# Optimization experiments

Hardware: AMD Instinct MI355X
Metric: run time of the kernel (lower is better)

Reference implementation:

```python
import jax, jax.numpy as jnp
import numpy as np

B, NMAX, T, FIN, H, K, OUT = 64, 256, 16, 3, 32, 8, 64
N = B * NMAX            # 16384 total nodes
EPG = 2048              # edges per graph
E = B * EPG             # 131072 edges
EPS = 1e-15


def gcn_conv(x, src, dst, ew, W, b):
    # x: [N, T, FIN] -> [N, T, H]; GCNConv: symmetric norm with self-loops (weight 1)
    xw = jnp.einsum('ntf,fh->nth', x, W)
    loops = jnp.arange(N, dtype=src.dtype)
    src_a = jnp.concatenate([src, loops])
    dst_a = jnp.concatenate([dst, loops])
    w_a = jnp.concatenate([ew, jnp.ones((N,), ew.dtype)])
    deg = jax.ops.segment_sum(w_a, dst_a, num_segments=N)
    dinv = jnp.where(deg > 0, jax.lax.rsqrt(deg), 0.0)
    norm = dinv[src_a] * w_a * dinv[dst_a]
    out = jax.ops.segment_sum(xw[src_a] * norm[:, None, None], dst_a, num_segments=N)
    return out + b


def dense_mincut_pool(x, adj, s):
    # x [B,T,Nc,H], adj [B,Nc,Nc], s [B,Nc,Kc]  (mask is all-True: equal-size graphs)
    s = jax.nn.softmax(s, axis=-1)
    kc = s.shape[-1]
    out = jnp.einsum('bnk,btnh->btkh', s, x)
    out_adj = jnp.einsum('bnk,bnm,bml->bkl', s, adj, s)
    mincut_num = jnp.trace(out_adj, axis1=-2, axis2=-1)
    d_flat = adj.sum(-1)
    mincut_den = jnp.einsum('bnk,bn,bnk->b', s, d_flat, s)
    mincut_loss = -jnp.mean(mincut_num / mincut_den)
    ss = jnp.einsum('bnk,bnl->bkl', s, s)
    i_s = jnp.eye(kc, dtype=x.dtype)
    ss_n = jnp.linalg.norm(ss, axis=(-2, -1), keepdims=True)
    ortho_loss = jnp.mean(jnp.linalg.norm(ss / ss_n - i_s / jnp.sqrt(kc), axis=(-2, -1)))
    out_adj = out_adj * (1.0 - i_s)  # zero diagonal
    d = jnp.sqrt(out_adj.sum(-1))[:, None, :] + EPS  # [B,1,K]
    out_adj = out_adj / d / jnp.swapaxes(d, 1, 2)
    return out, out_adj, mincut_loss, ortho_loss


def dense_graph_conv(x, adj, Wrel, brel, Wroot):
    # DenseGraphConv(aggr='add'): lin_rel(adj @ x) + lin_root(x)
    agg = jnp.einsum('bnm,btmh->btnh', adj, x)
    return jnp.einsum('btnh,ho->btno', agg, Wrel) + brel + jnp.einsum('btnh,ho->btno', x, Wroot)


def _forward(pos, edge_attr, W1, b1, Wp1, bp1, Wrel2, brel2, Wroot2, Wp2, bp2,
             Wrel3, brel3, Wroot3, Wp3, bp3, Wrel4, brel4, Wroot4, edge_src, edge_dst):
    x = jax.nn.relu(gcn_conv(pos, edge_src, edge_dst, edge_attr, W1, b1))  # [N,T,H]
    # to_dense_batch (equal-size graphs => reshape) then transpose(1,2)
    xd = x.reshape(B, NMAX, T, H).transpose(0, 2, 1, 3)  # [B,T,NMAX,H]
    gb = edge_src // NMAX
    adj = jnp.zeros((B, NMAX, NMAX), jnp.float32).at[gb, edge_src % NMAX, edge_dst % NMAX].add(1.0)
    s1 = jnp.tanh((jnp.einsum('btnh,hk->btnk', xd, Wp1) + bp1).mean(1))   # [B,NMAX,8K]
    x1, adj1, mc1, o1 = dense_mincut_pool(xd, adj, s1)
    x1 = dense_graph_conv(x1, adj1, Wrel2, brel2, Wroot2)
    s2 = jnp.tanh((jnp.einsum('btnh,hk->btnk', x1, Wp2) + bp2).mean(1))   # [B,8K,4K]
    x2, adj2, mc2, o2 = dense_mincut_pool(x1, adj1, s2)
    x2 = dense_graph_conv(x2, adj2, Wrel3, brel3, Wroot3)
    s3 = jnp.tanh((jnp.einsum('btnh,hk->btnk', x2, Wp3) + bp3).mean(1))   # [B,4K,K]
    x3, adj3, mc3, o3 = dense_mincut_pool(x2, adj2, s3)
    x3 = dense_graph_conv(x3, adj3, Wrel4, brel4, Wroot4)                 # [B,T,K,OUT]
    p1 = jax.nn.softmax(s1, -1)
    p2 = jax.nn.softmax(s2, -1)
    p3 = jax.nn.softmax(s3, -1)
    agg = jnp.einsum('bnk,bkl,blm->bnm', p1, p2, p3)                       # [B,NMAX,K]
    return x3, mc1 + mc2 + mc3, o1 + o2 + o3, agg


def setup_inputs():
    key = jax.random.key(0)
    ks = jax.random.split(key, 16)
    pos = jax.random.normal(ks[0], (N, T, FIN), jnp.float32)
    gid = jnp.repeat(jnp.arange(B, dtype=jnp.int32), EPG)
    sl = jax.random.randint(ks[1], (E,), 0, NMAX, jnp.int32)
    dl = jax.random.randint(ks[2], (E,), 0, NMAX, jnp.int32)
    edge_src = gid * NMAX + sl
    edge_dst = gid * NMAX + dl
    edge_attr = jax.random.uniform(ks[3], (E,), jnp.float32)

    def lin(k, i, o):
        return jax.random.normal(k, (i, o), jnp.float32) / np.sqrt(i)

    return dict(
        pos=pos, edge_attr=edge_attr, edge_src=edge_src, edge_dst=edge_dst,
        W1=lin(ks[4], FIN, H), b1=jnp.zeros((H,), jnp.float32),
        Wp1=lin(ks[5], H, 8 * K), bp1=jnp.zeros((8 * K,), jnp.float32),
        Wrel2=lin(ks[6], H, H), brel2=jnp.zeros((H,), jnp.float32), Wroot2=lin(ks[7], H, H),
        Wp2=lin(ks[8], H, 4 * K), bp2=jnp.zeros((4 * K,), jnp.float32),
        Wrel3=lin(ks[9], H, H), brel3=jnp.zeros((H,), jnp.float32), Wroot3=lin(ks[10], H, H),
        Wp3=lin(ks[11], H, K), bp3=jnp.zeros((K,), jnp.float32),
        Wrel4=lin(ks[12], H, OUT), brel4=jnp.zeros((OUT,), jnp.float32), Wroot4=lin(ks[13], H, OUT),
    )


def reference(pos, edge_attr, edge_src, edge_dst, W1, b1, Wp1, bp1, Wrel2, brel2, Wroot2,
              Wp2, bp2, Wrel3, brel3, Wroot3, Wp3, bp3, Wrel4, brel4, Wroot4):
    return _forward(pos, edge_attr, W1, b1, Wp1, bp1, Wrel2, brel2, Wroot2, Wp2, bp2,
                    Wrel3, brel3, Wroot3, Wp3, bp3, Wrel4, brel4, Wroot4, edge_src, edge_dst)
```

## Files before the change

kernel.cpp:

```cpp
#include <hip/hip_runtime.h>
#include <math.h>

#define NB 64
#define TC 16
#define HC 32
#define NNODES 16384
#define NEDGES 131072
#define EPG 2048
#define EPSV 1e-15f

static inline int GRID(int n) { return (n + 255) / 256; }

template<int V> struct Log2 { static constexpr int v = 1 + Log2<V/2>::v; };
template<> struct Log2<1> { static constexpr int v = 0; };

__device__ inline float blk_sum256(float v, float* rbuf) {
    for (int o = 32; o > 0; o >>= 1) v += __shfl_xor(v, o);
    __syncthreads();
    if ((threadIdx.x & 63) == 0) rbuf[threadIdx.x >> 6] = v;
    __syncthreads();
    return rbuf[0] + rbuf[1] + rbuf[2] + rbuf[3];
}

__device__ inline float blk_sum512(float v, float* rbuf) {
    for (int o = 32; o > 0; o >>= 1) v += __shfl_xor(v, o);
    __syncthreads();
    if ((threadIdx.x & 63) == 0) rbuf[threadIdx.x >> 6] = v;
    __syncthreads();
    float s = 0.f;
#pragma unroll
    for (int i = 0; i < 8; ++i) s += rbuf[i];
    return s;
}

__global__ __launch_bounds__(512) void k_front(
        const int* __restrict__ esrc, const int* __restrict__ edst,
        const float* __restrict__ ea, const float* __restrict__ pos,
        const float* __restrict__ W1, const float* __restrict__ b1,
        const float* __restrict__ Wp1, const float* __restrict__ bp1,
        float* __restrict__ z, float* __restrict__ dinv_g,
        float* __restrict__ p1, float* __restrict__ mc) {
    __shared__ float dinvs[256];
    __shared__ __align__(16) float as_[1152];
    __shared__ __align__(16) float bs[1536];
    __shared__ __align__(16) float zs[1536];
    __shared__ float xm[1024];
    __shared__ float s1[2048];
    __shared__ __align__(16) float wp[2048];
    __shared__ float W1s[96];
    __shared__ float b1s[32];
    __shared__ float bp1s[64];

    int bid = blockIdx.x;
    int b = (bid & 7) * 8 + (bid >> 6);
    int dtile = ((bid >> 3) & 7) * 32;
    int tid = threadIdx.x;
    if (bid == 0 && tid < 2) mc[tid] = 0.f;
    ((float4*)wp)[tid] = ((const float4*)Wp1)[tid];
    if (tid < 96) W1s[tid] = W1[tid];
    if (tid < 32) b1s[tid] = b1[tid];
    if (tid < 64) bp1s[tid] = bp1[tid];

    int ebase = b * EPG;
    int svr[4], dvr[4];
    float evr[4];
#pragma unroll
    for (int j = 0; j < 4; ++j) {
        int e = ebase + tid + j * 512;
        svr[j] = esrc[e] & 255;
        dvr[j] = edst[e] & 255;
        evr[j] = ea[e];
    }
    if (tid < 256) dinvs[tid] = 1.0f;
    __syncthreads();
#pragma unroll
    for (int j = 0; j < 4; ++j) atomicAdd(&dinvs[dvr[j]], evr[j]);
    __syncthreads();
    float dvv = 0.f;
    if (tid < 256) {
        float dg = dinvs[tid];
        dvv = (dg > 0.f) ? rsqrtf(dg) : 0.f;
    }
    __syncthreads();
    if (tid < 256) dinvs[tid] = dvv;
    __syncthreads();
    if (dtile == 0 && tid < 256) dinv_g[b * 256 + tid] = dinvs[tid];

    int d = tid >> 4, q = tid & 15;
    bool act = (q < 12);
    float4 acc = make_float4(0.f, 0.f, 0.f, 0.f);
    const float* pbase = pos + (size_t)b * 256 * 48;
    for (int s0 = 0; s0 < 256; s0 += 32) {
        for (int i = tid; i < 288; i += 512)
            ((float4*)as_)[i] = make_float4(0.f, 0.f, 0.f, 0.f);
        __syncthreads();
#pragma unroll
        for (int j = 0; j < 4; ++j) {
            int dr = dvr[j] - dtile, sc = svr[j] - s0;
            if ((unsigned)dr < 32u && (unsigned)sc < 32u)
                atomicAdd(&as_[dr * 36 + sc], evr[j]);
        }
        for (int i = tid; i < 384; i += 512) {
            int r = i / 12, c = i % 12;
            float4 v = *(const float4*)(pbase + (size_t)(s0 + r) * 48 + c * 4);
            float dd = dinvs[s0 + r];
            v.x *= dd; v.y *= dd; v.z *= dd; v.w *= dd;
            *(float4*)(bs + r * 48 + c * 4) = v;
        }
        __syncthreads();
        if (act) {
#pragma unroll 8
            for (int sp = 0; sp < 32; ++sp) {
                float a = as_[d * 36 + sp];
                float4 bv = *(const float4*)&bs[sp * 48 + q * 4];
                acc.x += a * bv.x;
                acc.y += a * bv.y;
                acc.z += a * bv.z;
                acc.w += a * bv.w;
            }
        }
        __syncthreads();
    }
    if (act) {
        float dd = dinvs[dtile + d];
        float d2 = dd * dd;
        size_t goff = ((size_t)(b * 256 + dtile + d)) * 48 + q * 4;
        float4 pv = *(const float4*)(pos + goff);
        float4 zv;
        zv.x = acc.x * dd; zv.y = acc.y * dd; zv.z = acc.z * dd; zv.w = acc.w * dd;
        *(float4*)(z + goff) = zv;
        float4 av;
        av.x = zv.x + pv.x * d2;
        av.y = zv.y + pv.y * d2;
        av.z = zv.z + pv.z * d2;
        av.w = zv.w + pv.w * d2;
        *(float4*)&zs[d * 48 + q * 4] = av;
    }
    __syncthreads();
    {
        int h = tid & 31, ng = tid >> 5;
        float w0 = W1s[h], w1 = W1s[32 + h], w2 = W1s[64 + h], bb = b1s[h];
#pragma unroll
        for (int j = 0; j < 2; ++j) {
            int nn = ng * 2 + j;
            float a = 0.f;
#pragma unroll
            for (int t = 0; t < 16; ++t) {
                const float* ap = &zs[nn * 48 + t * 3];
                float y = fmaxf(ap[0] * w0 + ap[1] * w1 + ap[2] * w2 + bb, 0.f);
                a += y;
            }
            xm[nn * 32 + h] = a * (1.0f / 16.0f);
        }
    }
    __syncthreads();
    for (int i = tid; i < 2048; i += 512) {
        int n = i >> 6, k = i & 63;
        float a = bp1s[k];
#pragma unroll 8
        for (int h2 = 0; h2 < 32; ++h2) a += xm[n * 32 + h2] * wp[h2 * 64 + k];
        s1[i] = tanhf(a);
    }
    __syncthreads();
    {
        int wid = tid >> 6, lane = tid & 63;
        for (int r0 = wid; r0 < 32; r0 += 8) {
            float v = s1[r0 * 64 + lane];
            float m = v;
            for (int o = 32; o > 0; o >>= 1) m = fmaxf(m, __shfl_xor(m, o));
            float e = expf(v - m);
            float s = e;
            for (int o = 32; o > 0; o >>= 1) s += __shfl_xor(s, o);
            p1[((size_t)b * 256 + dtile + r0) * 64 + lane] = e / s;
        }
    }
}

__global__ __launch_bounds__(256) void k_pool1f(
        const float* __restrict__ z, const float* __restrict__ pos,
        const float* __restrict__ dinv, const float* __restrict__ p1,
        const float* __restrict__ W1, const float* __restrict__ b1,
        float* __restrict__ X1A) {
    __shared__ __align__(16) float ps[4096];
    __shared__ __align__(16) float ys[4096];
    __shared__ float zc[384];
    __shared__ float pc[384];
    __shared__ float dv[64];
    __shared__ float W1s[96];
    __shared__ float b1s[32];
    int bid = blockIdx.x;
    int b = (bid & 7) * 8 + (bid >> 6);
    int t0 = ((bid >> 3) & 7) * 2;
    int tid = threadIdx.x;
    if (tid < 96) W1s[tid] = W1[tid];
    if (tid < 32) b1s[tid] = b1[tid];
    __syncthreads();
    int hh = tid & 31;
    float w0 = W1s[hh], w1 = W1s[32 + hh], w2 = W1s[64 + hh], bb = b1s[hh];
    int th = tid >> 7, r = tid & 127;
    int k0 = (r >> 3) * 4, h0 = (r & 7) * 4;
    float acc[4][4];
#pragma unroll
    for (int a = 0; a < 4; ++a)
#pragma unroll
        for (int c = 0; c < 4; ++c) acc[a][c] = 0.f;
    for (int n0 = 0; n0 < 256; n0 += 64) {
        for (int i = tid; i < 1024; i += 256)
            ((float4*)ps)[i] = ((const float4*)(p1 + ((size_t)b * 256 + n0) * 64))[i];
        if (tid < 192) {
            int n = tid / 3, c = tid % 3;
            size_t off = ((size_t)(b * 256 + n0 + n)) * 48 + t0 * 3 + c * 2;
            *(float2*)&zc[n * 6 + c * 2] = *(const float2*)(z + off);
            *(float2*)&pc[n * 6 + c * 2] = *(const float2*)(pos + off);
        }
        if (tid < 64) dv[tid] = dinv[b * 256 + n0 + tid];
        __syncthreads();
        int g = tid >> 5;
#pragma unroll
        for (int j = 0; j < 16; ++j) {
            int pidx = g * 16 + j;
            int t = pidx >> 6, nn = pidx & 63;
            float d2 = dv[nn] * dv[nn];
            const float* zp = &zc[nn * 6 + t * 3];
            const float* pp = &pc[nn * 6 + t * 3];
            float a0 = zp[0] + pp[0] * d2;
            float a1 = zp[1] + pp[1] * d2;
            float a2 = zp[2] + pp[2] * d2;
            ys[t * 2048 + nn * 32 + hh] = fmaxf(a0 * w0 + a1 * w1 + a2 * w2 + bb, 0.f);
        }
        __syncthreads();
#pragma unroll 4
        for (int n = 0; n < 64; ++n) {
            float4 kv4 = *(const float4*)&ps[n * 64 + k0];
            float4 xv4 = *(const float4*)&ys[th * 2048 + n * 32 + h0];
            float kv[4] = {kv4.x, kv4.y, kv4.z, kv4.w};
            float xv[4] = {xv4.x, xv4.y, xv4.z, xv4.w};
#pragma unroll
            for (int a = 0; a < 4; ++a)
#pragma unroll
                for (int c = 0; c < 4; ++c) acc[a][c] += kv[a] * xv[c];
        }
        __syncthreads();
    }
    float* ob = X1A + (((size_t)(b * 16 + t0 + th) * 64 + k0) * 32 + h0);
#pragma unroll
    for (int a = 0; a < 4; ++a) {
        float4 v = {acc[a][0], acc[a][1], acc[a][2], acc[a][3]};
        *(float4*)(ob + (size_t)a * 32) = v;
    }
}

__global__ void k_adjp2(const int* __restrict__ esrc, const int* __restrict__ edst,
                        const float* __restrict__ p, float* __restrict__ tmp,
                        float* __restrict__ dflat) {
    __shared__ __align__(16) float as_[32 * 260];
    __shared__ __align__(16) float ps[64 * 64];
    int bid = blockIdx.x;
    int b = (bid & 7) * 8 + (bid >> 6);
    int nt0 = ((bid >> 3) & 7) * 32;
    int tid = threadIdx.x;
    for (int i = tid; i < 32 * 260 / 4; i += 256)
        ((float4*)as_)[i] = make_float4(0.f, 0.f, 0.f, 0.f);
    __syncthreads();
    int ebase = b * EPG;
#pragma unroll
    for (int j = 0; j < 8; ++j) {
        int e = ebase + tid + j * 256;
        int sv = esrc[e] & 255;
        int nr = sv - nt0;
        if ((unsigned)nr < 32u)
            atomicAdd(&as_[nr * 260 + (edst[e] & 255)], 1.0f);
    }
    __syncthreads();
    int n = tid >> 3, l0 = (tid & 7) * 8;
    float acc[8];
#pragma unroll
    for (int j = 0; j < 8; ++j) acc[j] = 0.f;
    float rs = 0.f;
    for (int m0 = 0; m0 < 256; m0 += 64) {
        for (int i = tid; i < 64 * 64 / 4; i += 256)
            ((float4*)ps)[i] = ((const float4*)(p + ((size_t)b * 256 + m0) * 64))[i];
        __syncthreads();
#pragma unroll 4
        for (int m = 0; m < 64; ++m) {
            float av = as_[n * 260 + m0 + m];
            rs += av;
            float4 p0 = *(const float4*)&ps[m * 64 + l0];
            float4 p1v = *(const float4*)&ps[m * 64 + l0 + 4];
            acc[0] += av * p0.x; acc[1] += av * p0.y; acc[2] += av * p0.z; acc[3] += av * p0.w;
            acc[4] += av * p1v.x; acc[5] += av * p1v.y; acc[6] += av * p1v.z; acc[7] += av * p1v.w;
        }
        __syncthreads();
    }
#pragma unroll
    for (int j = 0; j < 8; ++j)
        tmp[((size_t)b * 256 + nt0 + n) * 64 + l0 + j] = acc[j];
    if ((tid & 7) == 0) dflat[(size_t)b * 256 + nt0 + n] = rs;
}

template<int NC, int KC, int NSPLIT, int KT, int LT>
__global__ void k_ssgp(const float* __restrict__ p, const float* __restrict__ tmp,
                       const float* __restrict__ dflat, float* __restrict__ G,
                       float* __restrict__ Gden) {
    constexpr int NCH = NC / NSPLIT;
    constexpr int LC = 2 * KC;
    constexpr int KQ = KC / 4;
    __shared__ __align__(16) float ab[NCH * LC];
    __shared__ float rbuf[4];
    int bid = blockIdx.x;
    int idx = bid >> 3;
    int b = (bid & 7) * 8 + idx / NSPLIT;
    int split = idx % NSPLIT;
    int n0 = split * NCH;
    int tid = threadIdx.x;
    const float* pb = p + ((size_t)b * NC + n0) * KC;
    const float* tb = tmp + ((size_t)b * NC + n0) * KC;
    const float* db = dflat + (size_t)b * NC + n0;
    for (int i = tid; i < NCH * KQ; i += 256) {
        int r = i / KQ, c = i % KQ;
        *(float4*)(ab + r * LC + c * 4) = ((const float4*)pb)[i];
        *(float4*)(ab + r * LC + KC + c * 4) = ((const float4*)tb)[i];
    }
    __syncthreads();
    float den = 0.f;
    for (int i = tid; i < NCH * KQ; i += 256) {
        int r = i / KQ, c = i % KQ;
        float4 v = *(const float4*)(ab + r * LC + c * 4);
        den += (v.x * v.x + v.y * v.y + v.z * v.z + v.w * v.w) * db[r];
    }
    int kt = tid >> 4, lt = tid & 15;
    int k0 = kt * KT, l0 = lt * LT;
    float acc[KT][LT];
#pragma unroll
    for (int r = 0; r < KT; ++r)
#pragma unroll
        for (int c = 0; c < LT; ++c) acc[r][c] = 0.f;
#pragma unroll 4
    for (int n = 0; n < NCH; ++n) {
        float kv[KT], lv[LT];
#pragma unroll
        for (int r = 0; r < KT; ++r) kv[r] = ab[n * LC + k0 + r];
#pragma unroll
        for (int c = 0; c < LT; ++c) lv[c] = ab[n * LC + l0 + c];
#pragma unroll
        for (int r = 0; r < KT; ++r)
#pragma unroll
            for (int c = 0; c < LT; ++c) acc[r][c] += kv[r] * lv[c];
    }
    float* Gb = G + ((size_t)split * NB + b) * (KC * LC);
#pragma unroll
    for (int r = 0; r < KT; ++r)
#pragma unroll
        for (int c = 0; c < LT; ++c)
            Gb[(k0 + r) * LC + l0 + c] = acc[r][c];
    float dt = blk_sum256(den, rbuf);
    if (tid == 0) Gden[(size_t)split * NB + b] = dt;
}

__global__ __launch_bounds__(512) void k_tail_a(
        const float* __restrict__ X1A, const float* __restrict__ GBUF1,
        const float* __restrict__ GDEN1, const float* __restrict__ p1,
        const float* __restrict__ Wrel2, const float* __restrict__ brel2,
        const float* __restrict__ Wroot2,
        const float* __restrict__ Wp2, const float* __restrict__ bp2,
        const float* __restrict__ Wrel3, const float* __restrict__ brel3,
        const float* __restrict__ Wroot3,
        const float* __restrict__ Wp3, const float* __restrict__ bp3,
        float* __restrict__ OADJ1G, float* __restrict__ P2G,
        float* __restrict__ OADJ2G, float* __restrict__ P3G,
        float* __restrict__ OADJ3G, float* __restrict__ outagg,
        float* __restrict__ mc_out, float* __restrict__ or_out) {
    __shared__ __align__(16) float lds[16160];
    float* P2     = lds;
    float* XM2    = lds + 2304;
    float* OADJ2L = lds + 4608;
    float* P3L    = lds + 5760;
    float* OADJ3L = lds + 6016;
    float* DF3    = lds + 6080;
    float* DVV    = lds + 6112;
    float* RBUF   = lds + 6152;
    float* OADJ1s = lds + 6160;
    float* S      = lds + 10512;
    float* DF2    = lds + 16080;

    int bid = blockIdx.x;
    int b = ((bid & 7) << 3) | (bid >> 3);
    int tid = threadIdx.x;

    {
        float* FS = lds;
        float* FO = lds + 4160;
        float* FD = lds + 8320;
        float* FR = lds + 8384;
#pragma unroll
        for (int j = 0; j < 8; ++j) {
            int i = tid + j * 512;
            int k = i >> 6, l = i & 63;
            float sv = 0.f, ov = 0.f;
#pragma unroll
            for (int s = 0; s < 4; ++s) {
                const float* Gb = GBUF1 + ((size_t)s * NB + b) * 8192;
                sv += Gb[k * 128 + l];
                ov += Gb[k * 128 + 64 + l];
            }
            FS[k * 65 + l] = sv;
            FO[k * 65 + l] = ov;
        }
        __syncthreads();
        float ssn2 = 0.f;
#pragma unroll
        for (int j = 0; j < 8; ++j) {
            int i = tid + j * 512;
            float v = FS[(i >> 6) * 65 + (i & 63)];
            ssn2 += v * v;
        }
        float num = 0.f;
        if (tid < 64) num = FO[tid * 65 + tid];
        float den_t = 0.f;
#pragma unroll
        for (int s = 0; s < 4; ++s) den_t += GDEN1[(size_t)s * NB + b];
        float ssn2_t = blk_sum512(ssn2, FR);
        float num_t = blk_sum512(num, FR);
        float inv = 1.0f / sqrtf(ssn2_t);
        float dk = rsqrtf(64.0f);
        float o2 = 0.f;
#pragma unroll
        for (int j = 0; j < 8; ++j) {
            int i = tid + j * 512;
            int k = i >> 6, l = i & 63;
            float v = FS[k * 65 + l] * inv - ((k == l) ? dk : 0.f);
            o2 += v * v;
        }
        float o2_t = blk_sum512(o2, FR);
        if (tid == 0) {
            atomicAdd(mc_out, -(num_t / den_t) * (1.0f / NB));
            atomicAdd(or_out, sqrtf(o2_t) * (1.0f / NB));
        }
        if (tid < 64) {
            float rs = 0.f;
            for (int l = 0; l < 64; ++l) rs += FO[tid * 65 + l];
            rs -= FO[tid * 65 + tid];
            FD[tid] = sqrtf(rs) + EPSV;
        }
        __syncthreads();
        float ov8[8];
#pragma unroll
        for (int j = 0; j < 8; ++j) {
            int i = tid + j * 512;
            int k = i >> 6, l = i & 63;
            ov8[j] = (k == l) ? 0.f : FO[k * 65 + l] / (FD[k] * FD[l]);
        }
        __syncthreads();
#pragma unroll
        for (int j = 0; j < 8; ++j) {
            int i = tid + j * 512;
            int k = i >> 6, l = i & 63;
            OADJ1s[k * 68 + l] = ov8[j];
            OADJ1G[(size_t)b * 4096 + i] = ov8[j];
        }
        __syncthreads();
        if (tid < 64) {
            float rs = 0.f;
            for (int l = 0; l < 64; ++l) rs += OADJ1s[tid * 68 + l];
            DF2[tid] = rs;
        }
        __syncthreads();
    }

    float* XM1A = S;
    for (int i = tid; i < 2048; i += 512) {
        float s = 0.f;
        for (int t = 0; t < 16; ++t) s += X1A[((size_t)b * 16 + t) * 2048 + i];
        XM1A[(i >> 5) * 36 + (i & 31)] = s * (1.0f / 16.0f);
    }
    {
        float* WR = P2;
        float* WO = P2 + 1024;
        for (int i = tid; i < 1024; i += 512) { WR[i] = Wrel2[i]; WO[i] = Wroot2[i]; }
        __syncthreads();
        float* C1 = S + 2304;
        int n = tid >> 3, j0 = (tid & 7) * 4;
        float a4[4] = {0, 0, 0, 0};
        for (int m = 0; m < 64; ++m) {
            float av = OADJ1s[n * 68 + m];
            float4 xv = *(const float4*)&XM1A[m * 36 + j0];
            a4[0] += av * xv.x; a4[1] += av * xv.y; a4[2] += av * xv.z; a4[3] += av * xv.w;
        }
        __syncthreads();
#pragma unroll
        for (int j = 0; j < 4; ++j) C1[n * 36 + j0 + j] = a4[j];
        __syncthreads();
        float o4[4];
#pragma unroll
        for (int j = 0; j < 4; ++j) o4[j] = brel2[j0 + j];
        for (int h = 0; h < 32; ++h) {
            float c1v = C1[n * 36 + h];
            float xav = XM1A[n * 36 + h];
            float4 wr = *(const float4*)&WR[h * 32 + j0];
            float4 wo = *(const float4*)&WO[h * 32 + j0];
            o4[0] += c1v * wr.x + xav * wo.x;
            o4[1] += c1v * wr.y + xav * wo.y;
            o4[2] += c1v * wr.z + xav * wo.z;
            o4[3] += c1v * wr.w + xav * wo.w;
        }
        __syncthreads();
#pragma unroll
        for (int j = 0; j < 4; ++j) XM2[n * 36 + j0 + j] = o4[j];
        __syncthreads();
    }
    {
        float* S2 = S;
        float* WP2s = S + 2048;
        for (int i = tid; i < 1024; i += 512) WP2s[i] = Wp2[i];
        __syncthreads();
        for (int i = tid; i < 2048; i += 512) {
            int n = i >> 5, k = i & 31;
            float a = bp2[k];
            for (int h = 0; h < 32; ++h) a += XM2[n * 36 + h] * WP2s[h * 32 + k];
            S2[i] = tanhf(a);
        }
        __syncthreads();
        int lane = tid & 31, rr = tid >> 5;
        for (int r0 = 0; r0 < 64; r0 += 16) {
            int row = r0 + rr;
            float v = S2[row * 32 + lane];
            float m = v;
            for (int o = 16; o > 0; o >>= 1) m = fmaxf(m, __shfl_xor(m, o, 32));
            float e = expf(v - m);
            float s = e;
            for (int o = 16; o > 0; o >>= 1) s += __shfl_xor(s, o, 32);
            P2[row * 36 + lane] = e / s;
        }
        __syncthreads();
        for (int i = tid; i < 2048; i += 512)
            P2G[(size_t)b * 2048 + i] = P2[(i >> 5) * 36 + (i & 31)];
    }
    float* TMP2 = S;
    {
        int n = tid >> 3, l0 = (tid & 7) * 4;
        float a4[4] = {0, 0, 0, 0};
        for (int m = 0; m < 64; ++m) {
            float av = OADJ1s[n * 68 + m];
            float4 pv = *(const float4*)&P2[m * 36 + l0];
            a4[0] += av * pv.x; a4[1] += av * pv.y; a4[2] += av * pv.z; a4[3] += av * pv.w;
        }
        __syncthreads();
#pragma unroll
        for (int j = 0; j < 4; ++j) TMP2[n * 36 + l0 + j] = a4[j];
        __syncthreads();
    }
    {
        float* GS = S + 2304;
        float* GO = S + 3360;
        int k = tid >> 4, l0 = (tid & 15) * 2;
        float as2[2] = {0, 0}, ao2[2] = {0, 0};
        for (int n = 0; n < 64; ++n) {
            float pv = P2[n * 36 + k];
            float2 lp = *(const float2*)&P2[n * 36 + l0];
            float2 lt = *(const float2*)&TMP2[n * 36 + l0];
            as2[0] += pv * lp.x; as2[1] += pv * lp.y;
            ao2[0] += pv * lt.x; ao2[1] += pv * lt.y;
        }
        GS[k * 33 + l0] = as2[0]; GS[k * 33 + l0 + 1] = as2[1];
        GO[k * 33 + l0] = ao2[0]; GO[k * 33 + l0 + 1] = ao2[1];
        __syncthreads();
        float den = 0.f;
        for (int i = tid; i < 2048; i += 512) {
            float pv = P2[(i >> 5) * 36 + (i & 31)];
            den += pv * pv * DF2[i >> 5];
        }
        float ssn2 = 0.f;
        for (int i = tid; i < 1024; i += 512) {
            float v = GS[(i >> 5) * 33 + (i & 31)];
            ssn2 += v * v;
        }
        float num = 0.f;
        if (tid < 32) num = GO[tid * 33 + tid];
        float den_t = blk_sum512(den, RBUF);
        float ssn2_t = blk_sum512(ssn2, RBUF);
        float num_t = blk_sum512(num, RBUF);
        float inv = 1.0f / sqrtf(ssn2_t);
        float dk = rsqrtf(32.0f);
        float o2 = 0.f;
        for (int i = tid; i < 1024; i += 512) {
            int kk = i >> 5, ll = i & 31;
            float v = GS[kk * 33 + ll] * inv - ((kk == ll) ? dk : 0.f);
            o2 += v * v;
        }
        float o2_t = blk_sum512(o2, RBUF);
        if (tid == 0) {
            atomicAdd(mc_out, -(num_t / den_t) * (1.0f / NB));
            atomicAdd(or_out, sqrtf(o2_t) * (1.0f / NB));
        }
        if (tid < 32) {
            float rs = 0.f;
            for (int l = 0; l < 32; ++l) rs += GO[tid * 33 + l];
            rs -= GO[tid * 33 + tid];
            DVV[tid] = sqrtf(rs) + EPSV;
        }
        __syncthreads();
        for (int i = tid; i < 1024; i += 512) {
            int kk = i >> 5, ll = i & 31;
            float v = (kk == ll) ? 0.f : GO[kk * 33 + ll] / (DVV[kk] * DVV[ll]);
            OADJ2L[kk * 36 + ll] = v;
            OADJ2G[(size_t)b * 1024 + i] = v;
        }
        __syncthreads();
        if (tid < 32) {
            float s = 0.f;
            for (int l = 0; l < 32; ++l) s += OADJ2L[tid * 36 + l];
            DF3[tid] = s;
        }
        __syncthreads();
    }
    float* XM2A = S;
    {
        int k = tid >> 4, h0 = (tid & 15) * 2;
        float a2[2] = {0, 0};
        for (int n = 0; n < 64; ++n) {
            float pv = P2[n * 36 + k];
            float2 xv = *(const float2*)&XM2[n * 36 + h0];
            a2[0] += pv * xv.x; a2[1] += pv * xv.y;
        }
        __syncthreads();
        XM2A[k * 36 + h0] = a2[0];
        XM2A[k * 36 + h0 + 1] = a2[1];
        __syncthreads();
    }
    float* XM2B = S + 4352;
    {
        float* WREL3s = S + 1152;
        float* WROOT3s = S + 2176;
        float* C1 = S + 3200;
        for (int i = tid; i < 1024; i += 512) {
            WREL3s[i] = Wrel3[i];
            WROOT3s[i] = Wroot3[i];
        }
        __syncthreads();
        int n = tid >> 4, j0 = (tid & 15) * 2;
        float a2[2] = {0, 0};
        for (int m = 0; m < 32; ++m) {
            float av = OADJ2L[n * 36 + m];
            float2 xv = *(const float2*)&XM2A[m * 36 + j0];
            a2[0] += av * xv.x; a2[1] += av * xv.y;
        }
        __syncthreads();
        C1[n * 36 + j0] = a2[0];
        C1[n * 36 + j0 + 1] = a2[1];
        __syncthreads();
        float o2v[2];
        o2v[0] = brel3[j0]; o2v[1] = brel3[j0 + 1];
        for (int h = 0; h < 32; ++h) {
            float c1v = C1[n * 36 + h];
            float xav = XM2A[n * 36 + h];
            float2 wr = *(const float2*)&WREL3s[h * 32 + j0];
            float2 wo = *(const float2*)&WROOT3s[h * 32 + j0];
            o2v[0] += c1v * wr.x + xav * wo.x;
            o2v[1] += c1v * wr.y + xav * wo.y;
        }
        __syncthreads();
        XM2B[n * 36 + j0] = o2v[0];
        XM2B[n * 36 + j0 + 1] = o2v[1];
        __syncthreads();
    }
    {
        float* WP3s = S;
        for (int i = tid; i < 256; i += 512) WP3s[i] = Wp3[i];
        __syncthreads();
        if (tid < 256) {
            int n = tid >> 3, kk = tid & 7;
            float a = bp3[kk];
            for (int h = 0; h < 32; ++h) a += XM2B[n * 36 + h] * WP3s[h * 8 + kk];
            float v = tanhf(a);
            float m = v;
            for (int o = 4; o > 0; o >>= 1) m = fmaxf(m, __shfl_xor(m, o, 8));
            float e = expf(v - m);
            float s = e;
            for (int o = 4; o > 0; o >>= 1) s += __shfl_xor(s, o, 8);
            P3L[n * 8 + kk] = e / s;
        }
        __syncthreads();
        if (tid < 256) P3G[(size_t)b * 256 + tid] = P3L[tid];
        __syncthreads();
    }
    {
        float* TMP3 = S;
        float* GS3 = S + 256;
        float* GO3 = S + 336;
        if (tid < 256) {
            int n = tid >> 3, l = tid & 7;
            float a = 0.f;
            for (int m = 0; m < 32; ++m) a += OADJ2L[n * 36 + m] * P3L[m * 8 + l];
            TMP3[n * 8 + l] = a;
        }
        __syncthreads();
        if (tid < 64) {
            int k = tid >> 3, ll = tid & 7;
            float accs = 0.f, acco = 0.f;
            for (int nn = 0; nn < 32; ++nn) {
                float pv = P3L[nn * 8 + k];
                accs += pv * P3L[nn * 8 + ll];
                acco += pv * TMP3[nn * 8 + ll];
            }
            GS3[k * 9 + ll] = accs;
            GO3[k * 9 + ll] = acco;
        }
        __syncthreads();
        float den = 0.f;
        if (tid < 256) {
            float pv = P3L[tid];
            den = pv * pv * DF3[tid >> 3];
        }
        float ssn2 = 0.f;
        if (tid < 64) {
            float v = GS3[(tid >> 3) * 9 + (tid & 7)];
            ssn2 = v * v;
        }
        float num = 0.f;
        if (tid < 8) num = GO3[tid * 9 + tid];
        float den_t = blk_sum512(den, RBUF);
        float ssn2_t = blk_sum512(ssn2, RBUF);
        float num_t = blk_sum512(num, RBUF);
        float inv = 1.0f / sqrtf(ssn2_t);
        float dk = rsqrtf(8.0f);
        float o2 = 0.f;
        if (tid < 64) {
            int k = tid >> 3, ll = tid & 7;
            float v = GS3[k * 9 + ll] * inv - ((k == ll) ? dk : 0.f);
            o2 = v * v;
        }
        float o2_t = blk_sum512(o2, RBUF);
        if (tid == 0) {
            atomicAdd(mc_out, -(num_t / den_t) * (1.0f / NB));
            atomicAdd(or_out, sqrtf(o2_t) * (1.0f / NB));
        }
        if (tid < 8) {
            float rs = 0.f;
            for (int ll = 0; ll < 8; ++ll) rs += GO3[tid * 9 + ll];
            rs -= GO3[tid * 9 + tid];
            DVV[32 + tid] = sqrtf(rs) + EPSV;
        }
        __syncthreads();
        if (tid < 64) {
            int k = tid >> 3, ll = tid & 7;
            float v = (k == ll) ? 0.f : GO3[k * 9 + ll] / (DVV[32 + k] * DVV[32 + ll]);
            OADJ3L[tid] = v;
            OADJ3G[(size_t)b * 64 + tid] = v;
        }
        __syncthreads();
    }
    {
        float* Q = S;
        {
            int k = tid >> 3, m = tid & 7;
            float a = 0.f;
            for (int l = 0; l < 32; ++l) a += P2[k * 36 + l] * P3L[l * 8 + m];
            Q[tid] = a;
        }
        __syncthreads();
        int row = tid >> 1, m0 = (tid & 1) * 4;
        const float* p1r = p1 + ((size_t)b * 256 + row) * 64;
        float a4[4] = {0, 0, 0, 0};
        for (int k = 0; k < 64; ++k) {
            float pv = p1r[k];
#pragma unroll
            for (int m = 0; m < 4; ++m) a4[m] += pv * Q[k * 8 + m0 + m];
        }
#pragma unroll
        for (int m = 0; m < 4; ++m)
            outagg[((size_t)b * 256 + row) * 8 + m0 + m] = a4[m];
    }
}

__global__ __launch_bounds__(256) void k_tail_b(
        const float* __restrict__ X1A, const float* __restrict__ oadj1,
        const float* __restrict__ P2G, const float* __restrict__ OADJ2G,
        const float* __restrict__ P3G, const float* __restrict__ OADJ3G,
        const float* __restrict__ Wrel2, const float* __restrict__ brel2,
        const float* __restrict__ Wroot2,
        const float* __restrict__ Wrel3, const float* __restrict__ brel3,
        const float* __restrict__ Wroot3,
        const float* __restrict__ Wrel4, const float* __restrict__ brel4,
        const float* __restrict__ Wroot4,
        float* __restrict__ outx) {
    __shared__ float A[13408];
    float* X1AT = A;
    float* OADJ1s = A + 2304;
    float* WrelS = A + 6656;
    float* WrootS = A + 7680;
    float* C1a = A + 8704;
    float* X1B = A + 11008;
    int bid = blockIdx.x;
    int idxg = bid >> 3;
    int t = idxg & 15;
    int b = (bid & 7) * 8 + (idxg >> 4);
    int bt = b * 16 + t;
    int tid = threadIdx.x;
    for (int i = tid; i < 2048; i += 256)
        X1AT[(i >> 5) * 36 + (i & 31)] = X1A[(size_t)bt * 2048 + i];
    for (int i = tid; i < 4096; i += 256)
        OADJ1s[(i >> 6) * 68 + (i & 63)] = oadj1[(size_t)b * 4096 + i];
    for (int i = tid; i < 1024; i += 256) {
        WrelS[i] = Wrel2[i];
        WrootS[i] = Wroot2[i];
    }
    __syncthreads();
    {
        int n = tid >> 2, j0 = (tid & 3) * 8;
        float a8[8];
#pragma unroll
        for (int j = 0; j < 8; ++j) a8[j] = 0.f;
        for (int m = 0; m < 64; ++m) {
            float av = OADJ1s[n * 68 + m];
            float4 x1 = *(const float4*)&X1AT[m * 36 + j0];
            float4 x2 = *(const float4*)&X1AT[m * 36 + j0 + 4];
            a8[0] += av * x1.x; a8[1] += av * x1.y; a8[2] += av * x1.z; a8[3] += av * x1.w;
            a8[4] += av * x2.x; a8[5] += av * x2.y; a8[6] += av * x2.z; a8[7] += av * x2.w;
        }
        __syncthreads();
#pragma unroll
        for (int j = 0; j < 8; ++j) C1a[n * 36 + j0 + j] = a8[j];
        __syncthreads();
        float o8[8];
#pragma unroll
        for (int j = 0; j < 8; ++j) o8[j] = brel2[j0 + j];
        for (int h = 0; h < 32; ++h) {
            float c1v = C1a[n * 36 + h];
            float xav = X1AT[n * 36 + h];
            float4 wr1 = *(const float4*)&WrelS[h * 32 + j0];
            float4 wr2 = *(const float4*)&WrelS[h * 32 + j0 + 4];
            float4 wo1 = *(const float4*)&WrootS[h * 32 + j0];
            float4 wo2 = *(const float4*)&WrootS[h * 32 + j0 + 4];
            o8[0] += c1v * wr1.x + xav * wo1.x; o8[1] += c1v * wr1.y + xav * wo1.y;
            o8[2] += c1v * wr1.z + xav * wo1.z; o8[3] += c1v * wr1.w + xav * wo1.w;
            o8[4] += c1v * wr2.x + xav * wo2.x; o8[5] += c1v * wr2.y + xav * wo2.y;
            o8[6] += c1v * wr2.z + xav * wo2.z; o8[7] += c1v * wr2.w + xav * wo2.w;
        }
        __syncthreads();
#pragma unroll
        for (int j = 0; j < 8; ++j) X1B[n * 36 + j0 + j] = o8[j];
        __syncthreads();
    }
    float* P2s = A;
    float* X2A = A + 2304;
    for (int i = tid; i < 2048; i += 256)
        P2s[(i >> 5) * 36 + (i & 31)] = P2G[(size_t)b * 2048 + i];
    __syncthreads();
    {
        int k = tid >> 3, h0 = (tid & 7) * 4;
        float a4[4] = {0, 0, 0, 0};
        for (int n = 0; n < 64; ++n) {
            float pv = P2s[n * 36 + k];
            float4 xv = *(const float4*)&X1B[n * 36 + h0];
            a4[0] += pv * xv.x; a4[1] += pv * xv.y; a4[2] += pv * xv.z; a4[3] += pv * xv.w;
        }
        __syncthreads();
        *(float4*)&X2A[k * 36 + h0] = make_float4(a4[0], a4[1], a4[2], a4[3]);
        __syncthreads();
    }
    float* OADJ2s = A + 3456;
    float* Wrel3s = A + 4608;
    float* Wroot3s = A + 5632;
    float* C1b = A + 6656;
    float* X2B = A + 7808;
    for (int i = tid; i < 1024; i += 256) {
        OADJ2s[(i >> 5) * 36 + (i & 31)] = OADJ2G[(size_t)b * 1024 + i];
        Wrel3s[i] = Wrel3[i];
        Wroot3s[i] = Wroot3[i];
    }
    __syncthreads();
    {
        int n = tid >> 3, j0 = (tid & 7) * 4;
        float a4[4] = {0, 0, 0, 0};
        for (int m = 0; m < 32; ++m) {
            float av = OADJ2s[n * 36 + m];
            float4 xv = *(const float4*)&X2A[m * 36 + j0];
            a4[0] += av * xv.x; a4[1] += av * xv.y; a4[2] += av * xv.z; a4[3] += av * xv.w;
        }
        __syncthreads();
        *(float4*)&C1b[n * 36 + j0] = make_float4(a4[0], a4[1], a4[2], a4[3]);
        __syncthreads();
        float o4[4];
#pragma unroll
        for (int j = 0; j < 4; ++j) o4[j] = brel3[j0 + j];
        for (int h = 0; h < 32; ++h) {
            float c1v = C1b[n * 36 + h];
            float xav = X2A[n * 36 + h];
            float4 wr = *(const float4*)&Wrel3s[h * 32 + j0];
            float4 wo = *(const float4*)&Wroot3s[h * 32 + j0];
            o4[0] += c1v * wr.x + xav * wo.x;
            o4[1] += c1v * wr.y + xav * wo.y;
            o4[2] += c1v * wr.z + xav * wo.z;
            o4[3] += c1v * wr.w + xav * wo.w;
        }
        __syncthreads();
        *(float4*)&X2B[n * 36 + j0] = make_float4(o4[0], o4[1], o4[2], o4[3]);
        __syncthreads();
    }
    float* P3s = A;
    float* X3A = A + 8960;
    P3s[tid] = P3G[(size_t)b * 256 + tid];
    __syncthreads();
    {
        int k = tid >> 5, h = tid & 31;
        float a = 0.f;
        for (int n = 0; n < 32; ++n) a += P3s[n * 8 + k] * X2B[n * 36 + h];
        __syncthreads();
        X3A[k * 36 + h] = a;
        __syncthreads();
    }
    {
        float* OADJ3s = A + 256;
        float* C3 = A + 320;
        float* Wrel4s = A + 9248;
        float* Wroot4s = A + 11296;
        if (tid < 64) OADJ3s[tid] = OADJ3G[(size_t)b * 64 + tid];
        for (int i = tid; i < 2048; i += 256) {
            Wrel4s[i] = Wrel4[i];
            Wroot4s[i] = Wroot4[i];
        }
        __syncthreads();
        int n = tid >> 5, h = tid & 31;
        float a = 0.f;
#pragma unroll
        for (int m = 0; m < 8; ++m) a += OADJ3s[n * 8 + m] * X3A[m * 36 + h];
        C3[n * 36 + h] = a;
        __syncthreads();
        int o0 = (tid & 31) * 2;
        float a0 = brel4[o0], a1 = brel4[o0 + 1];
        for (int hh = 0; hh < 32; ++hh) {
            float c3v = C3[n * 36 + hh];
            float x3v = X3A[n * 36 + hh];
            a0 += c3v * Wrel4s[hh * 64 + o0] + x3v * Wroot4s[hh * 64 + o0];
            a1 += c3v * Wrel4s[hh * 64 + o0 + 1] + x3v * Wroot4s[hh * 64 + o0 + 1];
        }
        float* ob = outx + ((size_t)bt * 8 + n) * 64 + o0;
        ob[0] = a0;
        ob[1] = a1;
    }
}


extern "C" void kernel_launch(void* const* d_in, const int* in_sizes, int n_in,
                              void* d_out, int out_size, void* d_ws, size_t ws_size,
                              hipStream_t stream) {
    const float* pos    = (const float*)d_in[0];
    const float* ea     = (const float*)d_in[1];
    const int*   esrc   = (const int*)d_in[2];
    const int*   edst   = (const int*)d_in[3];
    const float* W1     = (const float*)d_in[4];
    const float* b1     = (const float*)d_in[5];
    const float* Wp1    = (const float*)d_in[6];
    const float* bp1    = (const float*)d_in[7];
    const float* Wrel2  = (const float*)d_in[8];
    const float* brel2  = (const float*)d_in[9];
    const float* Wroot2 = (const float*)d_in[10];
    const float* Wp2    = (const float*)d_in[11];
    const float* bp2    = (const float*)d_in[12];
    const float* Wrel3  = (const float*)d_in[13];
    const float* brel3  = (const float*)d_in[14];
    const float* Wroot3 = (const float*)d_in[15];
    const float* Wp3    = (const float*)d_in[16];
    const float* bp3    = (const float*)d_in[17];
    const float* Wrel4  = (const float*)d_in[18];
    const float* brel4  = (const float*)d_in[19];
    const float* Wroot4 = (const float*)d_in[20];
    float* out = (float*)d_out;

    char* w = (char*)d_ws;
    float* TMP    = (float*)(w);
    float* GBUF1  = (float*)(w + 4194304);
    float* X1A    = (float*)(w + 12582912);
    float* Z      = (float*)(w + 20971520);
    float* P1     = (float*)(w + 25165824);
    float* DINV   = (float*)(w + 29360128);
    float* DFLAT  = (float*)(w + 29425664);
    float* GDEN1  = (float*)(w + 29507584);
    float* OADJ1  = (float*)(w + 29622272);
    float* P2G    = (float*)(w + 30670848);
    float* OADJ2G = (float*)(w + 31195136);
    float* P3G    = (float*)(w + 31457280);
    float* OADJ3G = (float*)(w + 31522816);
    float* MC     = out + 524288;

    k_front<<<NB * 8, 512, 0, stream>>>(esrc, edst, ea, pos, W1, b1, Wp1, bp1,
                                        Z, DINV, P1, MC);
    k_pool1f<<<NB * 8, 256, 0, stream>>>(Z, pos, DINV, P1, W1, b1, X1A);
    k_adjp2<<<NB * 8, 256, 0, stream>>>(esrc, edst, P1, TMP, DFLAT);
    k_ssgp<256, 64, 4, 4, 8><<<NB * 4, 256, 0, stream>>>(P1, TMP, DFLAT, GBUF1, GDEN1);
    k_tail_a<<<NB, 512, 0, stream>>>(X1A, GBUF1, GDEN1, P1,
                                     Wrel2, brel2, Wroot2, Wp2, bp2,
                                     Wrel3, brel3, Wroot3, Wp3, bp3,
                                     OADJ1, P2G, OADJ2G, P3G, OADJ3G,
                                     out + 524290, MC, MC + 1);
    k_tail_b<<<NB * TC, 256, 0, stream>>>(X1A, OADJ1, P2G, OADJ2G, P3G, OADJ3G,
                                          Wrel2, brel2, Wroot2,
                                          Wrel3, brel3, Wroot3,
                                          Wrel4, brel4, Wroot4, out);
}
```

Measured before the change: 147.9 us.

## Fuse adjacency-times-assignment kernel into Gram kernel, keeping intermediates in LDS

Merges k_adjp2 and k_ssgp into one kernel. Each block now builds the dense adjacency counts for its 64-node slice in two 32-row halves, computes adj@p into shared memory, and then forms the Gram product directly, so the TMP and DFLAT round trips through global memory and one launch go away. In exchange the grid shrinks from 512 to 256 blocks, each block runs the edge scan and adjacency matmul twice serially, and shared memory use per block grows, which may lower occupancy.

```diff
diff --git a/kernel.cpp b/kernel.cpp
--- a/kernel.cpp
+++ b/kernel.cpp
@@ -250,109 +250,98 @@
     }
 }
 
-__global__ void k_adjp2(const int* __restrict__ esrc, const int* __restrict__ edst,
-                        const float* __restrict__ p, float* __restrict__ tmp,
-                        float* __restrict__ dflat) {
-    __shared__ __align__(16) float as_[32 * 260];
+__global__ __launch_bounds__(256) void k_adjssg(
+        const int* __restrict__ esrc, const int* __restrict__ edst,
+        const float* __restrict__ p, float* __restrict__ G,
+        float* __restrict__ Gden) {
+    __shared__ __align__(16) float cnt[32 * 260];
     __shared__ __align__(16) float ps[64 * 64];
-    int bid = blockIdx.x;
-    int b = (bid & 7) * 8 + (bid >> 6);
-    int nt0 = ((bid >> 3) & 7) * 32;
-    int tid = threadIdx.x;
-    for (int i = tid; i < 32 * 260 / 4; i += 256)
-        ((float4*)as_)[i] = make_float4(0.f, 0.f, 0.f, 0.f);
-    __syncthreads();
-    int ebase = b * EPG;
-#pragma unroll
-    for (int j = 0; j < 8; ++j) {
-        int e = ebase + tid + j * 256;
-        int sv = esrc[e] & 255;
-        int nr = sv - nt0;
-        if ((unsigned)nr < 32u)
-            atomicAdd(&as_[nr * 260 + (edst[e] & 255)], 1.0f);
-    }
-    __syncthreads();
-    int n = tid >> 3, l0 = (tid & 7) * 8;
-    float acc[8];
-#pragma unroll
-    for (int j = 0; j < 8; ++j) acc[j] = 0.f;
-    float rs = 0.f;
-    for (int m0 = 0; m0 < 256; m0 += 64) {
-        for (int i = tid; i < 64 * 64 / 4; i += 256)
-            ((float4*)ps)[i] = ((const float4*)(p + ((size_t)b * 256 + m0) * 64))[i];
-        __syncthreads();
-#pragma unroll 4
-        for (int m = 0; m < 64; ++m) {
-            float av = as_[n * 260 + m0 + m];
-            rs += av;
-            float4 p0 = *(const float4*)&ps[m * 64 + l0];
-            float4 p1v = *(const float4*)&ps[m * 64 + l0 + 4];
-            acc[0] += av * p0.x; acc[1] += av * p0.y; acc[2] += av * p0.z; acc[3] += av * p0.w;
-            acc[4] += av * p1v.x; acc[5] += av * p1v.y; acc[6] += av * p1v.z; acc[7] += av * p1v.w;
-        }
-        __syncthreads();
-    }
-#pragma unroll
-    for (int j = 0; j < 8; ++j)
-        tmp[((size_t)b * 256 + nt0 + n) * 64 + l0 + j] = acc[j];
-    if ((tid & 7) == 0) dflat[(size_t)b * 256 + nt0 + n] = rs;
-}
-
-template<int NC, int KC, int NSPLIT, int KT, int LT>
-__global__ void k_ssgp(const float* __restrict__ p, const float* __restrict__ tmp,
-                       const float* __restrict__ dflat, float* __restrict__ G,
-                       float* __restrict__ Gden) {
-    constexpr int NCH = NC / NSPLIT;
-    constexpr int LC = 2 * KC;
-    constexpr int KQ = KC / 4;
-    __shared__ __align__(16) float ab[NCH * LC];
+    __shared__ __align__(16) float tmpL[64 * 64];
+    __shared__ float dfl[64];
     __shared__ float rbuf[4];
     int bid = blockIdx.x;
     int idx = bid >> 3;
-    int b = (bid & 7) * 8 + idx / NSPLIT;
-    int split = idx % NSPLIT;
-    int n0 = split * NCH;
+    int b = (bid & 7) * 8 + idx / 4;
+    int split = idx % 4;
+    int n0 = split * 64;
     int tid = threadIdx.x;
-    const float* pb = p + ((size_t)b * NC + n0) * KC;
-    const float* tb = tmp + ((size_t)b * NC + n0) * KC;
-    const float* db = dflat + (size_t)b * NC + n0;
-    for (int i = tid; i < NCH * KQ; i += 256) {
-        int r = i / KQ, c = i % KQ;
-        *(float4*)(ab + r * LC + c * 4) = ((const float4*)pb)[i];
-        *(float4*)(ab + r * LC + KC + c * 4) = ((const float4*)tb)[i];
-    }
+    int ebase = b * EPG;
+
+    for (int half = 0; half < 2; ++half) {
+        int nh0 = n0 + half * 32;
+        for (int i = tid; i < 2080; i += 256)
+            ((float4*)cnt)[i] = make_float4(0.f, 0.f, 0.f, 0.f);
+        __syncthreads();
+#pragma unroll
+        for (int j = 0; j < 8; ++j) {
+            int e = ebase + tid + j * 256;
+            int sv = esrc[e] & 255;
+            int nr = sv - nh0;
+            if ((unsigned)nr < 32u)
+                atomicAdd(&cnt[nr * 260 + (edst[e] & 255)], 1.0f);
+        }
+        __syncthreads();
+        int n = tid >> 3, l0 = (tid & 7) * 8;
+        float acc[8];
+#pragma unroll
+        for (int j = 0; j < 8; ++j) acc[j] = 0.f;
+        float rs = 0.f;
+        for (int m0 = 0; m0 < 256; m0 += 64) {
+            for (int i = tid; i < 1024; i += 256)
+                ((float4*)ps)[i] = ((const float4*)(p + ((size_t)b * 256 + m0) * 64))[i];
+            __syncthreads();
+#pragma unroll 4
+            for (int m = 0; m < 64; ++m) {
+                float av = cnt[n * 260 + m0 + m];
+                rs += av;
+                float4 p0 = *(const float4*)&ps[m * 64 + l0];
+                float4 p1v = *(const float4*)&ps[m * 64 + l0 + 4];
+                acc[0] += av * p0.x; acc[1] += av * p0.y; acc[2] += av * p0.z; acc[3] += av * p0.w;
+                acc[4] += av * p1v.x; acc[5] += av * p1v.y; acc[6] += av * p1v.z; acc[7] += av * p1v.w;
+            }
+            __syncthreads();
+        }
+#pragma unroll
+        for (int j = 0; j < 8; ++j)
+            tmpL[(half * 32 + n) * 64 + l0 + j] = acc[j];
+        if ((tid & 7) == 0) dfl[half * 32 + n] = rs;
+        __syncthreads();
+    }
+
+    for (int i = tid; i < 1024; i += 256)
+        ((float4*)ps)[i] = ((const float4*)(p + ((size_t)b * 256 + n0) * 64))[i];
     __syncthreads();
     float den = 0.f;
-    for (int i = tid; i < NCH * KQ; i += 256) {
-        int r = i / KQ, c = i % KQ;
-        float4 v = *(const float4*)(ab + r * LC + c * 4);
-        den += (v.x * v.x + v.y * v.y + v.z * v.z + v.w * v.w) * db[r];
+    for (int i = tid; i < 1024; i += 256) {
+        float4 v = ((const float4*)ps)[i];
+        den += (v.x * v.x + v.y * v.y + v.z * v.z + v.w * v.w) * dfl[i >> 4];
     }
     int kt = tid >> 4, lt = tid & 15;
-    int k0 = kt * KT, l0 = lt * LT;
-    float acc[KT][LT];
-#pragma unroll
-    for (int r = 0; r < KT; ++r)
-#pragma unroll
-        for (int c = 0; c < LT; ++c) acc[r][c] = 0.f;
+    int k0 = kt * 4, l0g = lt * 8;
+    const float* lsrc = (lt < 8) ? (ps + l0g) : (tmpL + (l0g - 64));
+    float accG[4][8];
+#pragma unroll
+    for (int r = 0; r < 4; ++r)
+#pragma unroll
+        for (int c = 0; c < 8; ++c) accG[r][c] = 0.f;
 #pragma unroll 4
-    for (int n = 0; n < NCH; ++n) {
-        float kv[KT], lv[LT];
-#pragma unroll
-        for (int r = 0; r < KT; ++r) kv[r] = ab[n * LC + k0 + r];
-#pragma unroll
-        for (int c = 0; c < LT; ++c) lv[c] = ab[n * LC + l0 + c];
-#pragma unroll
-        for (int r = 0; r < KT; ++r)
-#pragma unroll
-            for (int c = 0; c < LT; ++c) acc[r][c] += kv[r] * lv[c];
-    }
-    float* Gb = G + ((size_t)split * NB + b) * (KC * LC);
-#pragma unroll
-    for (int r = 0; r < KT; ++r)
-#pragma unroll
-        for (int c = 0; c < LT; ++c)
-            Gb[(k0 + r) * LC + l0 + c] = acc[r][c];
+    for (int nn = 0; nn < 64; ++nn) {
+        float kv[4], lv[8];
+#pragma unroll
+        for (int r = 0; r < 4; ++r) kv[r] = ps[nn * 64 + k0 + r];
+#pragma unroll
+        for (int c = 0; c < 8; ++c) lv[c] = lsrc[nn * 64 + c];
+#pragma unroll
+        for (int r = 0; r < 4; ++r)
+#pragma unroll
+            for (int c = 0; c < 8; ++c) accG[r][c] += kv[r] * lv[c];
+    }
+    float* Gb = G + ((size_t)split * NB + b) * 8192;
+#pragma unroll
+    for (int r = 0; r < 4; ++r)
+#pragma unroll
+        for (int c = 0; c < 8; ++c)
+            Gb[(k0 + r) * 128 + l0g + c] = accG[r][c];
     float dt = blk_sum256(den, rbuf);
     if (tid == 0) Gden[(size_t)split * NB + b] = dt;
 }
@@ -968,13 +957,11 @@
     float* out = (float*)d_out;
 
     char* w = (char*)d_ws;
-    float* TMP    = (float*)(w);
     float* GBUF1  = (float*)(w + 4194304);
     float* X1A    = (float*)(w + 12582912);
     float* Z      = (float*)(w + 20971520);
     float* P1     = (float*)(w + 25165824);
     float* DINV   = (float*)(w + 29360128);
-    float* DFLAT  = (float*)(w + 29425664);
     float* GDEN1  = (float*)(w + 29507584);
     float* OADJ1  = (float*)(w + 29622272);
     float* P2G    = (float*)(w + 30670848);
@@ -986,8 +973,7 @@
     k_front<<<NB * 8, 512, 0, stream>>>(esrc, edst, ea, pos, W1, b1, Wp1, bp1,
                                         Z, DINV, P1, MC);
     k_pool1f<<<NB * 8, 256, 0, stream>>>(Z, pos, DINV, P1, W1, b1, X1A);
-    k_adjp2<<<NB * 8, 256, 0, stream>>>(esrc, edst, P1, TMP, DFLAT);
-    k_ssgp<256, 64, 4, 4, 8><<<NB * 4, 256, 0, stream>>>(P1, TMP, DFLAT, GBUF1, GDEN1);
+    k_adjssg<<<NB * 4, 256, 0, stream>>>(esrc, edst, P1, GBUF1, GDEN1);
     k_tail_a<<<NB, 512, 0, stream>>>(X1A, GBUF1, GDEN1, P1,
                                      Wrel2, brel2, Wroot2, Wp2, bp2,
                                      Wrel3, brel3, Wroot3, Wp3, bp3,
```

Result: slower. 152.6 us (+3.2%).
